# Performance work log

Measured on AMD Instinct MI355X. Metric: run time of the kernel, lower is better.

## Reference

```python
import jax, jax.numpy as jnp
import numpy as np

# pars (match init_kwargs)
ALPHA, BETA = 0.9, 0.8            # synaptic / membrane decay (snn.Synaptic)
THRESHOLD = 1.0
BETA_PLUS, BETA_MINUS = 0.9, 0.9  # pre / post trace decay
A_PLUS, A_MINUS = 0.008, 0.0066   # STDP learning rates
W_MIN, W_MAX = 0.0, 1.0
NUM_STEPS, INPUT_SIZE, N_NEURONS = 256, 784, 512
SPIKE_RATE = 0.1                  # Bernoulli rate for the input spike train


def setup_inputs() -> dict:
    key = jax.random.key(0)
    k1, k2 = jax.random.split(key)
    # binary pre-synaptic spike train [num_steps, input_size]
    image = (jax.random.uniform(k1, (NUM_STEPS, INPUT_SIZE)) < SPIKE_RATE).astype(jnp.float32)
    # fc.weight, clamped into [w_min, w_max] as in __init__
    W = jax.random.uniform(k2, (N_NEURONS, INPUT_SIZE), minval=W_MIN, maxval=W_MAX)
    return {"image": image, "W": W}


def reference(image, W):
    """Faithful scan over time of: Linear -> Synaptic LIF (subtract reset) ->
    post-trace update -> classic STDP weight update with clamp.
    Returns (W_rec, spk_rec, mem_rec, syn_rec, post_rec) stacked over time."""
    dtype = image.dtype
    n = W.shape[0]
    d = image.shape[1]
    syn0 = jnp.zeros((n,), dtype)
    mem0 = jnp.zeros((n,), dtype)
    spk0 = jnp.zeros((n,), dtype)   # previous spike -> reset term
    post0 = jnp.zeros((n,), dtype)  # post-synaptic trace
    pre0 = jnp.zeros((d,), dtype)   # pre-synaptic trace (generate_traces: trace[0]=0)

    def step(carry, x_t):
        syn, mem, spk_prev, post, pre_tr, Wc = carry
        # fc (no bias)
        I = Wc @ x_t                                   # [n_neurons]
        # snntorch Synaptic, reset_mechanism='subtract' (reset from prev-step mem)
        syn = ALPHA * syn + I
        mem = BETA * mem + syn - spk_prev * THRESHOLD
        spk = (mem > THRESHOLD).astype(dtype)
        # post-synaptic trace update (before STDP, as in forward)
        post = BETA_MINUS * post + spk
        # classic STDP
        ltp = A_PLUS * jnp.outer(spk, pre_tr)          # [n, d]
        ltd = A_MINUS * jnp.outer(post, x_t)           # [n, d]
        Wn = jnp.clip(Wc + ltp - ltd, W_MIN, W_MAX)
        # pre-trace recurrence: trace[t+1] = beta_plus*trace[t] + image[t]
        pre_new = BETA_PLUS * pre_tr + x_t
        return (syn, mem, spk, post, pre_new, Wn), (spk, mem, syn, post, Wn)

    _, (spk_rec, mem_rec, syn_rec, post_rec, W_rec) = jax.lax.scan(
        step, (syn0, mem0, spk0, post0, pre0, W), image)
    return W_rec, spk_rec, mem_rec, syn_rec, post_rec
```

## Files before the change

kernel.cpp:

```cpp
#include <hip/hip_runtime.h>
#include <stdint.h>

#define NUM_STEPS  256
#define INPUT_SIZE 784
#define N_NEURONS  512

typedef float    v4f __attribute__((ext_vector_type(4)));
typedef uint16_t v4h __attribute__((ext_vector_type(4)));

__device__ __forceinline__ float bf2f(unsigned short u) {
    union { uint32_t i; float f; } v; v.i = ((uint32_t)u) << 16; return v.f;
}
__device__ __forceinline__ unsigned short f2bf(float f) {
    union { float f; uint32_t i; } v; v.f = f;
    uint32_t x = v.i;
    return (unsigned short)((x + 0x7fffu + ((x >> 16) & 1u)) >> 16);
}

template <bool F32>
__device__ __forceinline__ void ld_chunk(const void* __restrict__ base, size_t elem, float* d) {
    if constexpr (F32) {
        const v4f v = *(const v4f*)((const float*)base + elem);
        d[0] = v.x; d[1] = v.y; d[2] = v.z; d[3] = v.w;
    } else {
        const v4h v = *(const v4h*)((const unsigned short*)base + elem);
        d[0] = bf2f(v.x); d[1] = bf2f(v.y); d[2] = bf2f(v.z); d[3] = bf2f(v.w);
    }
}

template <bool F32>
__device__ __forceinline__ void st_chunk_nt(void* __restrict__ base, size_t elem, const float* s) {
    if constexpr (F32) {
        v4f v; v.x = s[0]; v.y = s[1]; v.z = s[2]; v.w = s[3];
        __builtin_nontemporal_store(v, (v4f*)((float*)base + elem));
    } else {
        v4h v; v.x = f2bf(s[0]); v.y = f2bf(s[1]); v.z = f2bf(s[2]); v.w = f2bf(s[3]);
        __builtin_nontemporal_store(v, (v4h*)((unsigned short*)base + elem));
    }
}

template <bool F32>
__device__ void scan_run(const void* __restrict__ img_v,
                         const void* __restrict__ W_v,
                         void* __restrict__ out_v,
                         uint2 (&msk)[64][64],
                         float (&sbuf)[2][64][4])
{
    const int tid  = threadIdx.x;
    const int wid  = tid >> 6;
    const int lane = tid & 63;
    const int row  = (blockIdx.x << 1) | wid;
    const bool has4 = lane < 4;

    const size_t WREC = (size_t)NUM_STEPS * N_NEURONS * INPUT_SIZE;
    const size_t SREC = (size_t)NUM_STEPS * N_NEURONS;

    size_t cofs[4];
    cofs[0] = (size_t)(lane      ) * 4;
    cofs[1] = (size_t)(lane +  64) * 4;
    cofs[2] = (size_t)(lane + 128) * 4;
    cofs[3] = (size_t)(192 + lane) * 4;

    for (int i = wid; i < 64; i += 2) {
        uint32_t lo = 0, hi = 0;
        #pragma unroll
        for (int s = 0; s < 4; ++s) {
            const int t = 4 * i + s;
            float a[4][4] = {};
            const size_t xb = (size_t)t * INPUT_SIZE;
            ld_chunk<F32>(img_v, xb + cofs[0], a[0]);
            ld_chunk<F32>(img_v, xb + cofs[1], a[1]);
            ld_chunk<F32>(img_v, xb + cofs[2], a[2]);
            if (has4) ld_chunk<F32>(img_v, xb + cofs[3], a[3]);
            uint32_t m = 0;
            #pragma unroll
            for (int c = 0; c < 4; ++c)
                #pragma unroll
                for (int j = 0; j < 4; ++j)
                    m |= (uint32_t)(a[c][j] != 0.0f) << (4 * c + j);
            if      (s == 0) lo  = m;
            else if (s == 1) lo |= m << 16;
            else if (s == 2) hi  = m;
            else             hi |= m << 16;
        }
        msk[i][lane] = make_uint2(lo, hi);
    }

    float wb0[16], wb1[16], wb2[16], wb3[16], p[16];
    #pragma unroll
    for (int k = 0; k < 16; ++k) { wb0[k] = 0.f; wb1[k] = 0.f; wb2[k] = 0.f; wb3[k] = 0.f; p[k] = 0.f; }
    {
        const size_t wbase = (size_t)row * INPUT_SIZE;
        ld_chunk<F32>(W_v, wbase + cofs[0], &wb0[0]);
        ld_chunk<F32>(W_v, wbase + cofs[1], &wb0[4]);
        ld_chunk<F32>(W_v, wbase + cofs[2], &wb0[8]);
        if (has4) ld_chunk<F32>(W_v, wbase + cofs[3], &wb0[12]);
    }

    __syncthreads();

    float syn = 0.f, mem = 0.f, spk_prev = 0.f, post = 0.f;
    int t = 0;

#define STEP(WI, WO, MB) do {                                                   \
        const uint32_t mb_ = (MB);                                              \
        float xf[16];                                                           \
        _Pragma("unroll")                                                       \
        for (int k = 0; k < 16; ++k) xf[k] = ((mb_ >> k) & 1u) ? 1.0f : 0.0f;   \
                                        \
        float g[8];                                                             \
        _Pragma("unroll")                                                       \
        for (int k = 0; k < 8; ++k)                                             \
            g[k] = WI[2*k] * xf[2*k] + WI[2*k+1] * xf[2*k+1];                   \
        const float h0_ = (g[0] + g[1]) + (g[2] + g[3]);                        \
        const float h1_ = (g[4] + g[5]) + (g[6] + g[7]);                        \
        float partial = h0_ + h1_;                                              \
        _Pragma("unroll")                                                       \
        for (int off = 1; off < 64; off <<= 1)                                  \
            partial += __shfl_xor(partial, off, 64);                            \
                       \
        syn = 0.9f * syn + partial;                                             \
        mem = 0.8f * mem + syn - spk_prev;                                      \
        const float spk = (mem > 1.0f) ? 1.0f : 0.0f;                           \
        post = 0.9f * post + spk;                                               \
        const float ap = 0.008f * spk, am = 0.0066f * post;                     \
        \
        _Pragma("unroll")                                                       \
        for (int k = 0; k < 16; ++k)                                            \
            WO[k] = fminf(fmaxf(WI[k] + ap * p[k] - am * xf[k], 0.0f), 1.0f);   \
        const size_t r_  = (size_t)t * N_NEURONS + row;                         \
        const size_t ob_ = r_ * INPUT_SIZE;                                     \
        st_chunk_nt<F32>(out_v, ob_ + cofs[0], &WO[0]);                         \
        st_chunk_nt<F32>(out_v, ob_ + cofs[1], &WO[4]);                         \
        st_chunk_nt<F32>(out_v, ob_ + cofs[2], &WO[8]);                         \
        if (has4) st_chunk_nt<F32>(out_v, ob_ + cofs[3], &WO[12]);              \
        if (lane == 0) {                                                        \
            v4f sv_; sv_.x = spk; sv_.y = mem; sv_.z = syn; sv_.w = post;       \
            *(v4f*)&sbuf[wid][t & 63][0] = sv_;                                 \
        }                                                                       \
        _Pragma("unroll")                                                       \
        for (int k = 0; k < 16; ++k) p[k] = 0.9f * p[k] + xf[k];                \
        spk_prev = spk; ++t;                                                    \
    } while (0)

    for (int i = 0; i < 64; ++i) {
        const uint2 mp = msk[i][lane];
        STEP(wb0, wb1, mp.x & 0xFFFFu);
        STEP(wb1, wb2, mp.x >> 16);
        STEP(wb2, wb3, mp.y & 0xFFFFu);
        STEP(wb3, wb0, mp.y >> 16);
        if ((i & 15) == 15) {
            const int t0 = (i - 15) * 4;
            const v4f sv = *(const v4f*)&sbuf[wid][lane][0];
            const size_t rr = (size_t)(t0 + lane) * N_NEURONS + row;
            if constexpr (F32) {
                float* out = (float*)out_v;
                out[WREC + 0 * SREC + rr] = sv.x;
                out[WREC + 1 * SREC + rr] = sv.y;
                out[WREC + 2 * SREC + rr] = sv.z;
                out[WREC + 3 * SREC + rr] = sv.w;
            } else {
                unsigned short* out = (unsigned short*)out_v;
                out[WREC + 0 * SREC + rr] = f2bf(sv.x);
                out[WREC + 1 * SREC + rr] = f2bf(sv.y);
                out[WREC + 2 * SREC + rr] = f2bf(sv.z);
                out[WREC + 3 * SREC + rr] = f2bf(sv.w);
            }
        }
    }
#undef STEP
}

__global__ __launch_bounds__(128) void snn_row_scan_kernel(
    const void* __restrict__ img,
    const void* __restrict__ W,
    void* __restrict__ out)
{
    __shared__ uint2 msk[64][64];
    __shared__ float sbuf[2][64][4];

    const unsigned short* w16 = (const unsigned short*)W;
    bool f32 = false;
    for (int i = 0; i < 128; ++i) f32 |= (w16[i] > 0x3F80u);
    if (f32) scan_run<true >(img, W, out, msk, sbuf);
    else     scan_run<false>(img, W, out, msk, sbuf);
}

extern "C" void kernel_launch(void* const* d_in, const int* in_sizes, int n_in,
                              void* d_out, int out_size, void* d_ws, size_t ws_size,
                              hipStream_t stream) {
    (void)in_sizes; (void)n_in; (void)d_ws; (void)ws_size; (void)out_size;
    snn_row_scan_kernel<<<dim3(N_NEURONS / 2), dim3(128), 0, stream>>>(d_in[0], d_in[1], d_out);
}
```

Measured before the change: 557.9 us.

## Split scan into serial neuron-state phase and parallel weight-record store phase

Phase 1 still runs the per-row recurrence over time, including the weight update, but no longer writes the W_rec history. It stores spk/mem/syn/post, and optionally a full-precision post copy in workspace. A second kernel with 2048 blocks recomputes each weight trajectory from the recorded spk/post and the input masks, then streams W_rec with nontemporal stores. This moves the dominant output write out of the serial 256-block scan and spreads it across many more blocks. The cost is recomputing the weight updates, an extra kernel launch, and a dependence on bf16-rounded spk/post values when no workspace is provided.

```diff
diff --git a/kernel.cpp b/kernel.cpp
--- a/kernel.cpp
+++ b/kernel.cpp
@@ -39,10 +39,18 @@
     }
 }
 
+__device__ __forceinline__ bool sniff_f32(const void* W) {
+    const unsigned short* w16 = (const unsigned short*)W;
+    bool f32 = false;
+    for (int i = 0; i < 128; ++i) f32 |= (w16[i] > 0x3F80u);
+    return f32;
+}
+
 template <bool F32>
 __device__ void scan_run(const void* __restrict__ img_v,
                          const void* __restrict__ W_v,
                          void* __restrict__ out_v,
+                         float* __restrict__ ws_post,
                          uint2 (&msk)[64][64],
                          float (&sbuf)[2][64][4])
 {
@@ -86,15 +94,15 @@
         msk[i][lane] = make_uint2(lo, hi);
     }
 
-    float wb0[16], wb1[16], wb2[16], wb3[16], p[16];
+    float w[16], p[16];
     #pragma unroll
-    for (int k = 0; k < 16; ++k) { wb0[k] = 0.f; wb1[k] = 0.f; wb2[k] = 0.f; wb3[k] = 0.f; p[k] = 0.f; }
+    for (int k = 0; k < 16; ++k) { w[k] = 0.f; p[k] = 0.f; }
     {
         const size_t wbase = (size_t)row * INPUT_SIZE;
-        ld_chunk<F32>(W_v, wbase + cofs[0], &wb0[0]);
-        ld_chunk<F32>(W_v, wbase + cofs[1], &wb0[4]);
-        ld_chunk<F32>(W_v, wbase + cofs[2], &wb0[8]);
-        if (has4) ld_chunk<F32>(W_v, wbase + cofs[3], &wb0[12]);
+        ld_chunk<F32>(W_v, wbase + cofs[0], &w[0]);
+        ld_chunk<F32>(W_v, wbase + cofs[1], &w[4]);
+        ld_chunk<F32>(W_v, wbase + cofs[2], &w[8]);
+        if (has4) ld_chunk<F32>(W_v, wbase + cofs[3], &w[12]);
     }
 
     __syncthreads();
@@ -102,38 +110,29 @@
     float syn = 0.f, mem = 0.f, spk_prev = 0.f, post = 0.f;
     int t = 0;
 
-#define STEP(WI, WO, MB) do {                                                   \
+#define STEP(MB) do {                                                           \
         const uint32_t mb_ = (MB);                                              \
         float xf[16];                                                           \
         _Pragma("unroll")                                                       \
         for (int k = 0; k < 16; ++k) xf[k] = ((mb_ >> k) & 1u) ? 1.0f : 0.0f;   \
-                                        \
         float g[8];                                                             \
         _Pragma("unroll")                                                       \
         for (int k = 0; k < 8; ++k)                                             \
-            g[k] = WI[2*k] * xf[2*k] + WI[2*k+1] * xf[2*k+1];                   \
+            g[k] = w[2*k] * xf[2*k] + w[2*k+1] * xf[2*k+1];                     \
         const float h0_ = (g[0] + g[1]) + (g[2] + g[3]);                        \
         const float h1_ = (g[4] + g[5]) + (g[6] + g[7]);                        \
         float partial = h0_ + h1_;                                              \
         _Pragma("unroll")                                                       \
         for (int off = 1; off < 64; off <<= 1)                                  \
             partial += __shfl_xor(partial, off, 64);                            \
-                       \
         syn = 0.9f * syn + partial;                                             \
         mem = 0.8f * mem + syn - spk_prev;                                      \
         const float spk = (mem > 1.0f) ? 1.0f : 0.0f;                           \
         post = 0.9f * post + spk;                                               \
         const float ap = 0.008f * spk, am = 0.0066f * post;                     \
-        \
         _Pragma("unroll")                                                       \
         for (int k = 0; k < 16; ++k)                                            \
-            WO[k] = fminf(fmaxf(WI[k] + ap * p[k] - am * xf[k], 0.0f), 1.0f);   \
-        const size_t r_  = (size_t)t * N_NEURONS + row;                         \
-        const size_t ob_ = r_ * INPUT_SIZE;                                     \
-        st_chunk_nt<F32>(out_v, ob_ + cofs[0], &WO[0]);                         \
-        st_chunk_nt<F32>(out_v, ob_ + cofs[1], &WO[4]);                         \
-        st_chunk_nt<F32>(out_v, ob_ + cofs[2], &WO[8]);                         \
-        if (has4) st_chunk_nt<F32>(out_v, ob_ + cofs[3], &WO[12]);              \
+            w[k] = fminf(fmaxf(w[k] + ap * p[k] - am * xf[k], 0.0f), 1.0f);     \
         if (lane == 0) {                                                        \
             v4f sv_; sv_.x = spk; sv_.y = mem; sv_.z = syn; sv_.w = post;       \
             *(v4f*)&sbuf[wid][t & 63][0] = sv_;                                 \
@@ -145,10 +144,10 @@
 
     for (int i = 0; i < 64; ++i) {
         const uint2 mp = msk[i][lane];
-        STEP(wb0, wb1, mp.x & 0xFFFFu);
-        STEP(wb1, wb2, mp.x >> 16);
-        STEP(wb2, wb3, mp.y & 0xFFFFu);
-        STEP(wb3, wb0, mp.y >> 16);
+        STEP(mp.x & 0xFFFFu);
+        STEP(mp.x >> 16);
+        STEP(mp.y & 0xFFFFu);
+        STEP(mp.y >> 16);
         if ((i & 15) == 15) {
             const int t0 = (i - 15) * 4;
             const v4f sv = *(const v4f*)&sbuf[wid][lane][0];
@@ -166,29 +165,107 @@
                 out[WREC + 2 * SREC + rr] = f2bf(sv.z);
                 out[WREC + 3 * SREC + rr] = f2bf(sv.w);
             }
+            if (ws_post) ws_post[rr] = sv.w;
         }
     }
 #undef STEP
 }
 
-__global__ __launch_bounds__(128) void snn_row_scan_kernel(
+__global__ __launch_bounds__(128) void snn_phase1_kernel(
     const void* __restrict__ img,
     const void* __restrict__ W,
-    void* __restrict__ out)
+    void* __restrict__ out,
+    float* __restrict__ ws_post)
 {
     __shared__ uint2 msk[64][64];
     __shared__ float sbuf[2][64][4];
-
-    const unsigned short* w16 = (const unsigned short*)W;
-    bool f32 = false;
-    for (int i = 0; i < 128; ++i) f32 |= (w16[i] > 0x3F80u);
-    if (f32) scan_run<true >(img, W, out, msk, sbuf);
-    else     scan_run<false>(img, W, out, msk, sbuf);
+    if (sniff_f32(W)) scan_run<true >(img, W, out, ws_post, msk, sbuf);
+    else              scan_run<false>(img, W, out, ws_post, msk, sbuf);
+}
+
+template <bool F32>
+__device__ void store_run(const void* __restrict__ img_v,
+                          const void* __restrict__ W_v,
+                          void* __restrict__ out_v,
+                          const float* __restrict__ ws_post,
+                          uint8_t (&msk8)[NUM_STEPS][64],
+                          float (&apam)[NUM_STEPS][2])
+{
+    const int lane = threadIdx.x;
+    const int row  = blockIdx.x >> 2;
+    const int q    = blockIdx.x & 3;
+    const bool act = lane < 49;
+    const int  col = (196 * q + 4 * lane);
+
+    const size_t WREC = (size_t)NUM_STEPS * N_NEURONS * INPUT_SIZE;
+    const size_t SREC = (size_t)NUM_STEPS * N_NEURONS;
+
+    for (int k = lane; k < NUM_STEPS; k += 64) {
+        const size_t rr = (size_t)k * N_NEURONS + row;
+        float spk, post;
+        if constexpr (F32) {
+            const float* o = (const float*)out_v;
+            spk  = o[WREC + 0 * SREC + rr];
+            post = o[WREC + 3 * SREC + rr];
+        } else {
+            const unsigned short* o = (const unsigned short*)out_v;
+            spk  = bf2f(o[WREC + 0 * SREC + rr]);
+            post = bf2f(o[WREC + 3 * SREC + rr]);
+        }
+        if (ws_post) post = ws_post[rr];
+        apam[k][0] = 0.008f  * spk;
+        apam[k][1] = 0.0066f * post;
+    }
+
+    if (act) {
+        for (int t = 0; t < NUM_STEPS; ++t) {
+            float a[4];
+            ld_chunk<F32>(img_v, (size_t)t * INPUT_SIZE + col, a);
+            uint32_t m = 0;
+            #pragma unroll
+            for (int j = 0; j < 4; ++j) m |= (uint32_t)(a[j] != 0.0f) << j;
+            msk8[t][lane] = (uint8_t)m;
+        }
+    }
+
+    float w[4] = {0.f, 0.f, 0.f, 0.f}, p[4] = {0.f, 0.f, 0.f, 0.f};
+    if (act) ld_chunk<F32>(W_v, (size_t)row * INPUT_SIZE + col, w);
+
+    #pragma unroll 4
+    for (int t = 0; t < NUM_STEPS; ++t) {
+        const uint32_t m = msk8[t][lane];
+        const float ap = apam[t][0], am = apam[t][1];
+        float x[4];
+        #pragma unroll
+        for (int j = 0; j < 4; ++j) x[j] = ((m >> j) & 1u) ? 1.0f : 0.0f;
+        #pragma unroll
+        for (int j = 0; j < 4; ++j)
+            w[j] = fminf(fmaxf(w[j] + ap * p[j] - am * x[j], 0.0f), 1.0f);
+        if (act)
+            st_chunk_nt<F32>(out_v, ((size_t)t * N_NEURONS + row) * INPUT_SIZE + col, w);
+        #pragma unroll
+        for (int j = 0; j < 4; ++j) p[j] = 0.9f * p[j] + x[j];
+    }
+}
+
+__global__ __launch_bounds__(64) void snn_phase2_kernel(
+    const void* __restrict__ img,
+    const void* __restrict__ W,
+    void* __restrict__ out,
+    const float* __restrict__ ws_post)
+{
+    __shared__ uint8_t msk8[NUM_STEPS][64];
+    __shared__ float   apam[NUM_STEPS][2];
+    if (sniff_f32(W)) store_run<true >(img, W, out, ws_post, msk8, apam);
+    else              store_run<false>(img, W, out, ws_post, msk8, apam);
 }
 
 extern "C" void kernel_launch(void* const* d_in, const int* in_sizes, int n_in,
                               void* d_out, int out_size, void* d_ws, size_t ws_size,
                               hipStream_t stream) {
-    (void)in_sizes; (void)n_in; (void)d_ws; (void)ws_size; (void)out_size;
-    snn_row_scan_kernel<<<dim3(N_NEURONS / 2), dim3(128), 0, stream>>>(d_in[0], d_in[1], d_out);
-}
+    (void)in_sizes; (void)n_in; (void)out_size;
+    float* ws_post = (d_ws && ws_size >= (size_t)NUM_STEPS * N_NEURONS * sizeof(float))
+                   ? (float*)d_ws : nullptr;
+    snn_phase1_kernel<<<dim3(N_NEURONS / 2), dim3(128), 0, stream>>>(d_in[0], d_in[1], d_out, ws_post);
+    snn_phase2_kernel<<<dim3(N_NEURONS * 4), dim3(64),  0, stream>>>(d_in[0], d_in[1], d_out, ws_post);
+}
```

Result: slower. 681.8 us (+22.2%).
